# Performance work log

Measured on AMD Instinct MI355X. Metric: run time of the kernel, lower is better.

Reference implementation:

```python
import jax, jax.numpy as jnp
import numpy as np

B, T, C = 4, 2048, 1024
N_HEAD = 16
HEAD_DIM = C // N_HEAD

def setup_inputs() -> dict:
    key = jax.random.key(0)
    k1, k2, k3 = jax.random.split(key, 3)
    x = jax.random.normal(k1, (B, T, C), dtype=jnp.float32)
    # nn.Linear(C, 3C, bias=False): weight [3C, C], y = x @ W.T
    w_qkv = jax.random.normal(k2, (3 * C, C), dtype=jnp.float32) * (1.0 / np.sqrt(C))
    w_proj = jax.random.normal(k3, (C, C), dtype=jnp.float32) * (1.0 / np.sqrt(C))
    return {"x": x, "w_qkv": w_qkv, "w_proj": w_proj}

def reference(x, w_qkv, w_proj):
    Bx, Tx, Cx = x.shape
    qkv = x @ w_qkv.T  # [B,T,3C]
    q, k, v = jnp.split(qkv, 3, axis=-1)
    def heads(t):
        return t.reshape(Bx, Tx, N_HEAD, HEAD_DIM).transpose(0, 2, 1, 3)  # [B,H,T,D]
    q, k, v = heads(q), heads(k), heads(v)
    scale = HEAD_DIM ** -0.5
    att = jnp.einsum('bhtd,bhsd->bhts', q, k) * scale  # [B,H,T,T]
    causal = jnp.tril(jnp.ones((Tx, Tx), dtype=bool))
    att = jnp.where(causal[None, None], att, -jnp.inf)
    att = jax.nn.softmax(att, axis=-1)
    y = jnp.einsum('bhts,bhsd->bhtd', att, v)  # [B,H,T,D]
    y = y.transpose(0, 2, 1, 3).reshape(Bx, Tx, Cx)
    return y @ w_proj.T
```

## Files before the change

### kernel.cpp

```cpp
#include <hip/hip_runtime.h>
#include <hip/hip_bf16.h>

typedef __attribute__((ext_vector_type(8))) short bf16x8;
typedef __attribute__((ext_vector_type(4))) float f32x4;
typedef __attribute__((ext_vector_type(4))) unsigned short ushort4v;
typedef __attribute__((ext_vector_type(2))) unsigned uint2v;

__device__ __forceinline__ unsigned short f2bf(float f) {
  union { float f; unsigned u; } v; v.f = f;
  unsigned r = v.u + 0x7FFFu + ((v.u >> 16) & 1u);
  return (unsigned short)(r >> 16);
}

__device__ __forceinline__ unsigned pack_bf2(float lo, float hi) {
  __hip_bfloat162 h = __float22bfloat162_rn(make_float2(lo, hi));
  union { __hip_bfloat162 h; unsigned u; } cv; cv.h = h; return cv.u;
}

__device__ __forceinline__ void gll16(const void* g, void* l) {
  __builtin_amdgcn_global_load_lds((const __attribute__((address_space(1))) void*)g,
                                   (__attribute__((address_space(3))) void*)l, 16, 0, 0);
}

#define MFMA16(a, b, c) __builtin_amdgcn_mfma_f32_16x16x32_bf16((a), (b), (c), 0, 0, 0)

__global__ void cvt_f32_bf16(const float* __restrict__ s, unsigned short* __restrict__ d, int n) {
  int i = (blockIdx.x * blockDim.x + threadIdx.x) * 4;
  if (i >= n) return;
  float4 f = *(const float4*)(s + i);
  ushort4v r;
  r[0] = f2bf(f.x); r[1] = f2bf(f.y); r[2] = f2bf(f.z); r[3] = f2bf(f.w);
  *(ushort4v*)(d + i) = r;
}

template<int EPI>
__global__ __launch_bounds__(512, 1)
void gemm8(const unsigned short* __restrict__ A,
           const unsigned short* __restrict__ B,
           unsigned short* __restrict__ obf,
           float* __restrict__ of32,
           int M, int N, int K) {
  extern __shared__ unsigned short lds[];
  const int tid = threadIdx.x, wid = tid >> 6, lane = tid & 63;
  const int c = lane & 15, g = lane >> 4;
  const int wr = wid >> 1, wc = wid & 1;
  const int nbn = N >> 7;
  const int nwg = gridDim.x;
  const int wg = (blockIdx.x & 7) * (nwg >> 3) + (blockIdx.x >> 3);
  const int m0 = (wg / nbn) * 256, n0 = (wg % nbn) * 128;
  const int NT = K >> 6;
  const size_t rb = (size_t)K * 2;
  const int sw = (c & 7) << 4;

  const int r8 = lane >> 3;
  const char* Ag = (const char*)A + (size_t)(m0 + r8) * rb + (((lane & 7) ^ r8) * 16);
  const char* Bg = (const char*)B + (size_t)(n0 + r8) * rb + (((lane & 7) ^ r8) * 16);

  auto stageA = [&](int t, int par) {
#pragma unroll
    for (int j = 0; j < 4; ++j) {
      int ch = wid * 4 + j;
      gll16(Ag + (size_t)(ch * 8) * rb + t * 128, lds + par * 16384 + ch * 512);
    }
  };
  auto stageB = [&](int t, int par) {
#pragma unroll
    for (int j = 0; j < 2; ++j) {
      int ch = wid * 2 + j;
      gll16(Bg + (size_t)(ch * 8) * rb + t * 128, lds + 32768 + par * 8192 + ch * 512);
    }
  };

  f32x4 acc[4][4];
#pragma unroll
  for (int i = 0; i < 4; ++i)
#pragma unroll
    for (int j = 0; j < 4; ++j) acc[i][j] = f32x4{0.f, 0.f, 0.f, 0.f};

  stageA(0, 0); stageB(0, 0); stageA(1, 1); stageB(1, 1);
  asm volatile("s_waitcnt vmcnt(4)" ::: "memory");
  __builtin_amdgcn_s_barrier();

  for (int t = 0; t < NT; ++t) {
    const int cur = t & 1;
    const char* Ac = (const char*)(lds + cur * 16384);
    const char* Bc = (const char*)(lds + 32768 + cur * 8192);
    bf16x8 af[4][2], bf0[2][2];
#pragma unroll
    for (int mi = 0; mi < 4; ++mi) {
      int arow = wr * 64 + mi * 16 + c;
#pragma unroll
      for (int kk = 0; kk < 2; ++kk)
        af[mi][kk] = *(const bf16x8*)(Ac + arow * 128 + ((kk * 64 + g * 16) ^ sw));
    }
#pragma unroll
    for (int ni = 0; ni < 2; ++ni) {
      int brow = wc * 64 + ni * 16 + c;
#pragma unroll
      for (int kk = 0; kk < 2; ++kk)
        bf0[ni][kk] = *(const bf16x8*)(Bc + brow * 128 + ((kk * 64 + g * 16) ^ sw));
    }
    if (t + 1 < NT) stageB(t + 1, cur ^ 1);
    __builtin_amdgcn_s_barrier();
    asm volatile("s_waitcnt lgkmcnt(0)" ::: "memory");
    __builtin_amdgcn_sched_barrier(0);
    __builtin_amdgcn_s_setprio(1);
#pragma unroll
    for (int kk = 0; kk < 2; ++kk)
#pragma unroll
      for (int mi = 0; mi < 4; ++mi)
#pragma unroll
        for (int ni = 0; ni < 2; ++ni)
          acc[mi][ni] = MFMA16(bf0[ni][kk], af[mi][kk], acc[mi][ni]);
    __builtin_amdgcn_s_setprio(0);
    __builtin_amdgcn_s_barrier();
    bf16x8 bf1[2][2];
#pragma unroll
    for (int ni = 0; ni < 2; ++ni) {
      int brow = wc * 64 + (ni + 2) * 16 + c;
#pragma unroll
      for (int kk = 0; kk < 2; ++kk)
        bf1[ni][kk] = *(const bf16x8*)(Bc + brow * 128 + ((kk * 64 + g * 16) ^ sw));
    }
    if (t + 2 < NT) stageA(t + 2, cur);
    __builtin_amdgcn_s_barrier();
    asm volatile("s_waitcnt lgkmcnt(0)" ::: "memory");
    __builtin_amdgcn_sched_barrier(0);
    __builtin_amdgcn_s_setprio(1);
#pragma unroll
    for (int kk = 0; kk < 2; ++kk)
#pragma unroll
      for (int mi = 0; mi < 4; ++mi)
#pragma unroll
        for (int ni = 0; ni < 2; ++ni)
          acc[mi][ni + 2] = MFMA16(bf1[ni][kk], af[mi][kk], acc[mi][ni + 2]);
    __builtin_amdgcn_s_setprio(0);
    if (t + 2 < NT) { asm volatile("s_waitcnt vmcnt(4)" ::: "memory"); }
    else            { asm volatile("s_waitcnt vmcnt(0)" ::: "memory"); }
    __builtin_amdgcn_s_barrier();
  }

#pragma unroll
  for (int mi = 0; mi < 4; ++mi) {
    int mg = m0 + wr * 64 + mi * 16 + c;
    if (EPI == 0) {
      int bb = mg >> 11, tt = mg & 2047;
      size_t rowbase = ((size_t)(bb * 16) * 2048 + tt) * 64;
#pragma unroll
      for (int ni = 0; ni < 4; ++ni) {
        int ng = n0 + wc * 64 + ni * 16 + g * 4;
        int which = ng >> 10, rem = ng & 1023;
        int hh = rem >> 6, dd = rem & 63;
        uint2v pk;
        pk[0] = pack_bf2(acc[mi][ni][0], acc[mi][ni][1]);
        pk[1] = pack_bf2(acc[mi][ni][2], acc[mi][ni][3]);
        *(uint2v*)(obf + (size_t)which * 8388608u + rowbase + (size_t)hh * 131072 + dd) = pk;
      }
    } else {
      float* orow = of32 + (size_t)mg * N + n0 + wc * 64 + g * 4;
#pragma unroll
      for (int ni = 0; ni < 4; ++ni)
        *(f32x4*)(orow + ni * 16) = acc[mi][ni];
    }
  }
}

__global__ __launch_bounds__(256, 6)
void attn_fwd(const unsigned short* __restrict__ qb,
              const unsigned short* __restrict__ kb,
              const unsigned short* __restrict__ vb,
              unsigned short* __restrict__ yb) {
  __shared__ unsigned short Kt[64 * 64];
  __shared__ unsigned short Vt[64 * 64];
  __shared__ unsigned short Pl[4 * 16 * 72];
  const int tid = threadIdx.x, w = tid >> 6, lane = tid & 63;
  const int c = lane & 15, g = lane >> 4;
  const int bh = blockIdx.x & 63;
  const int qt = 31 - (blockIdx.x >> 6);
  const int q0 = qt * 64;
  const int b = bh >> 4, h = bh & 15;
  const size_t hb = (size_t)bh * 131072;
  const float GAM = 0.125f * 1.44269504089f;

  const unsigned short* qp = qb + hb + (size_t)(q0 + w * 16 + c) * 64;
  bf16x8 qf0 = *(const bf16x8*)(qp + g * 8);
  bf16x8 qf1 = *(const bf16x8*)(qp + 32 + g * 8);

  f32x4 yacc[4];
#pragma unroll
  for (int i = 0; i < 4; ++i) yacc[i] = f32x4{0.f, 0.f, 0.f, 0.f};
  float mrun = -1e30f, lsum = 0.f;
  unsigned short* pw = Pl + w * (16 * 72);

  for (int kv = 0; kv <= qt; ++kv) {
    const int kv0 = kv * 64;
    const bool diag = (kv == qt);
    if (kv) __syncthreads();
#pragma unroll
    for (int r = 0; r < 2; ++r) {
      int chunk = w * 2 + r;
      int row = chunk * 8 + (lane >> 3);
      int bo = (lane & 7) * 16;
      int sbo = bo ^ ((row & 7) << 4);
      gll16((const char*)(kb + hb + (size_t)(kv0 + row) * 64) + sbo, Kt + chunk * 512);
    }
    {
      int kv2 = (lane & 31) * 2;
      int dblk = w * 16 + (lane >> 5) * 8;
      const unsigned short* vp = vb + hb + (size_t)(kv0 + kv2) * 64 + dblk;
      bf16x8 r0 = *(const bf16x8*)(vp);
      bf16x8 r1 = *(const bf16x8*)(vp + 64);
#pragma unroll
      for (int i = 0; i < 8; ++i) {
        int d = dblk + i;
        unsigned pk2 = ((unsigned)(unsigned short)r0[i]) | (((unsigned)(unsigned short)r1[i]) << 16);
        *(unsigned*)(Vt + d * 64 + (kv2 ^ ((d & 7) << 3))) = pk2;
      }
    }
    __syncthreads();

    f32x4 sacc[4];
#pragma unroll
    for (int nt = 0; nt < 4; ++nt) sacc[nt] = f32x4{0.f, 0.f, 0.f, 0.f};
#pragma unroll
    for (int kk = 0; kk < 2; ++kk)
#pragma unroll
      for (int nt = 0; nt < 4; ++nt) {
        int row = nt * 16 + c;
        bf16x8 kf = *(const bf16x8*)(Kt + row * 64 + ((kk * 32 + g * 8) ^ ((row & 7) << 3)));
        sacc[nt] = MFMA16(kf, (kk ? qf1 : qf0), sacc[nt]);
      }

    if (diag) {
      int ql = w * 16 + c;
#pragma unroll
      for (int nt = 0; nt < 4; ++nt)
#pragma unroll
        for (int r = 0; r < 4; ++r)
          if (nt * 16 + g * 4 + r > ql) sacc[nt][r] = -1e30f;
    }

    float m0 = -1e30f;
#pragma unroll
    for (int nt = 0; nt < 4; ++nt) {
      float a = fmaxf(fmaxf(sacc[nt][0], sacc[nt][1]), fmaxf(sacc[nt][2], sacc[nt][3]));
      m0 = fmaxf(m0, a);
    }
    m0 = fmaxf(m0, __shfl_xor(m0, 16));
    m0 = fmaxf(m0, __shfl_xor(m0, 32));

    if (__any(m0 > mrun + 32.0f)) {
      float mnew = fmaxf(mrun, m0);
      float corr = __builtin_amdgcn_exp2f(GAM * (mrun - mnew));
      lsum *= corr;
#pragma unroll
      for (int dt = 0; dt < 4; ++dt) yacc[dt] *= corr;
      mrun = mnew;
    }

    float bexp = -GAM * mrun;
    float psum = 0.f;
#pragma unroll
    for (int nt = 0; nt < 4; ++nt) {
      float p0 = __builtin_amdgcn_exp2f(fmaf(sacc[nt][0], GAM, bexp));
      float p1 = __builtin_amdgcn_exp2f(fmaf(sacc[nt][1], GAM, bexp));
      float p2 = __builtin_amdgcn_exp2f(fmaf(sacc[nt][2], GAM, bexp));
      float p3 = __builtin_amdgcn_exp2f(fmaf(sacc[nt][3], GAM, bexp));
      psum += (p0 + p1) + (p2 + p3);
      uint2v pkv;
      pkv[0] = pack_bf2(p0, p1);
      pkv[1] = pack_bf2(p2, p3);
      *(uint2v*)(pw + c * 72 + nt * 16 + g * 4) = pkv;
    }
    lsum += psum;

#pragma unroll
    for (int kk = 0; kk < 2; ++kk) {
      bf16x8 pb = *(const bf16x8*)(pw + c * 72 + kk * 32 + g * 8);
#pragma unroll
      for (int dt = 0; dt < 4; ++dt) {
        int n = dt * 16 + c;
        bf16x8 vf = *(const bf16x8*)(Vt + n * 64 + ((kk * 32 + g * 8) ^ ((n & 7) << 3)));
        yacc[dt] = MFMA16(vf, pb, yacc[dt]);
      }
    }
  }

  lsum += __shfl_xor(lsum, 16);
  lsum += __shfl_xor(lsum, 32);
  float inv = 1.0f / lsum;
  int row = q0 + w * 16 + c;
  unsigned short* yp = yb + ((size_t)(b * 2048 + row)) * 1024 + h * 64;
#pragma unroll
  for (int dt = 0; dt < 4; ++dt) {
    uint2v pkv;
    pkv[0] = pack_bf2(yacc[dt][0] * inv, yacc[dt][1] * inv);
    pkv[1] = pack_bf2(yacc[dt][2] * inv, yacc[dt][3] * inv);
    *(uint2v*)(yp + dt * 16 + g * 4) = pkv;
  }
}

extern "C" void kernel_launch(void* const* d_in, const int* in_sizes, int n_in,
                              void* d_out, int out_size, void* d_ws, size_t ws_size,
                              hipStream_t stream) {
  const float* x     = (const float*)d_in[0];
  const float* wqkv  = (const float*)d_in[1];
  const float* wproj = (const float*)d_in[2];
  float* out = (float*)d_out;

  unsigned short* ws     = (unsigned short*)d_ws;
  unsigned short* xb     = ws;
  unsigned short* wqkvb  = xb + 8388608;
  unsigned short* wprojb = wqkvb + 3145728;
  unsigned short* qkvb   = wprojb + 1048576;
  unsigned short* yb     = qkvb + 3 * 8388608;

  cvt_f32_bf16<<<8192, 256, 0, stream>>>(x, xb, 8388608);
  cvt_f32_bf16<<<3072, 256, 0, stream>>>(wqkv, wqkvb, 3145728);
  cvt_f32_bf16<<<1024, 256, 0, stream>>>(wproj, wprojb, 1048576);

  gemm8<0><<<768, 512, 98304, stream>>>(xb, wqkvb, qkvb, nullptr, 8192, 3072, 1024);
  attn_fwd<<<2048, 256, 0, stream>>>(qkvb, qkvb + 8388608, qkvb + 2 * 8388608, yb);
  gemm8<1><<<256, 512, 98304, stream>>>(yb, wprojb, nullptr, out, 8192, 1024, 1024);
}
```

Measured before the change: 179.5 us.

## Make QKV GEMM persistent with cross-tile prefetch; compute softmax denominator via MFMA

The QKV GEMM becomes a persistent kernel: 256 blocks each process three output tiles and prefetch the next tile's first K-slices during the current tile's tail, hiding the prologue and epilogue. The attention kernel drops the scalar row-sum of probabilities. It instead runs one extra MFMA against a ones matrix in LDS to get the softmax denominator, and XOR-swizzles the P buffer instead of padding it. This trades some extra MFMA work and an LDS ones tile for fewer VALU adds and shuffles, and the persistent GEMM risks imbalance since 768 tiles over 256 CUs is even only if all CUs are free.

```diff
diff --git a/kernel.cpp b/kernel.cpp
--- a/kernel.cpp
+++ b/kernel.cpp
@@ -33,9 +33,9 @@
   *(ushort4v*)(d + i) = r;
 }
 
-template<int EPI>
+template<int EPI, int RPB>
 __global__ __launch_bounds__(512, 1)
-void gemm8(const unsigned short* __restrict__ A,
+void gemmp(const unsigned short* __restrict__ A,
            const unsigned short* __restrict__ B,
            unsigned short* __restrict__ obf,
            float* __restrict__ of32,
@@ -45,29 +45,30 @@
   const int c = lane & 15, g = lane >> 4;
   const int wr = wid >> 1, wc = wid & 1;
   const int nbn = N >> 7;
-  const int nwg = gridDim.x;
-  const int wg = (blockIdx.x & 7) * (nwg >> 3) + (blockIdx.x >> 3);
-  const int m0 = (wg / nbn) * 256, n0 = (wg % nbn) * 128;
+  const int swzbid = (blockIdx.x & 7) * (gridDim.x >> 3) + (blockIdx.x >> 3);
   const int NT = K >> 6;
   const size_t rb = (size_t)K * 2;
   const int sw = (c & 7) << 4;
 
-  const int r8 = lane >> 3;
-  const char* Ag = (const char*)A + (size_t)(m0 + r8) * rb + (((lane & 7) ^ r8) * 16);
-  const char* Bg = (const char*)B + (size_t)(n0 + r8) * rb + (((lane & 7) ^ r8) * 16);
-
-  auto stageA = [&](int t, int par) {
+  const int srow = lane >> 3;
+  const int sslot = (lane & 7) ^ srow;
+  const char* Abase = (const char*)A;
+  const char* Bbase = (const char*)B;
+
+  auto stageA = [&](int m0p, int kt, int par) {
+    const char* Agp = Abase + (size_t)(m0p + srow) * rb + sslot * 16 + kt * 128;
 #pragma unroll
     for (int j = 0; j < 4; ++j) {
       int ch = wid * 4 + j;
-      gll16(Ag + (size_t)(ch * 8) * rb + t * 128, lds + par * 16384 + ch * 512);
+      gll16(Agp + (size_t)(ch * 8) * rb, lds + par * 16384 + ch * 512);
     }
   };
-  auto stageB = [&](int t, int par) {
+  auto stageB = [&](int n0p, int kt, int par) {
+    const char* Bgp = Bbase + (size_t)(n0p + srow) * rb + sslot * 16 + kt * 128;
 #pragma unroll
     for (int j = 0; j < 2; ++j) {
       int ch = wid * 2 + j;
-      gll16(Bg + (size_t)(ch * 8) * rb + t * 128, lds + 32768 + par * 8192 + ch * 512);
+      gll16(Bgp + (size_t)(ch * 8) * rb, lds + 32768 + par * 8192 + ch * 512);
     }
   };
 
@@ -77,91 +78,116 @@
 #pragma unroll
     for (int j = 0; j < 4; ++j) acc[i][j] = f32x4{0.f, 0.f, 0.f, 0.f};
 
-  stageA(0, 0); stageB(0, 0); stageA(1, 1); stageB(1, 1);
+  int m0c = (swzbid / nbn) * 256, n0c = (swzbid % nbn) * 128;
+
+  stageA(m0c, 0, 0); stageB(n0c, 0, 0); stageA(m0c, 1, 1); stageB(n0c, 1, 1);
   asm volatile("s_waitcnt vmcnt(4)" ::: "memory");
   __builtin_amdgcn_s_barrier();
 
-  for (int t = 0; t < NT; ++t) {
-    const int cur = t & 1;
-    const char* Ac = (const char*)(lds + cur * 16384);
-    const char* Bc = (const char*)(lds + 32768 + cur * 8192);
-    bf16x8 af[4][2], bf0[2][2];
+  for (int p = 0; p < RPB; ++p) {
+    int m0n = 0, n0n = 0;
+    const bool morep = (p + 1 < RPB);
+    if (morep) {
+      int tile = (p + 1) * gridDim.x + swzbid;
+      m0n = (tile / nbn) * 256; n0n = (tile % nbn) * 128;
+    }
+    for (int t = 0; t < NT; ++t) {
+      const int par = t & 1;
+      const char* Ac = (const char*)(lds + par * 16384);
+      const char* Bc = (const char*)(lds + 32768 + par * 8192);
+      bf16x8 af[4][2], bf0[2][2];
+#pragma unroll
+      for (int mi = 0; mi < 4; ++mi) {
+        int arow = wr * 64 + mi * 16 + c;
+#pragma unroll
+        for (int kk = 0; kk < 2; ++kk)
+          af[mi][kk] = *(const bf16x8*)(Ac + arow * 128 + ((kk * 64 + g * 16) ^ sw));
+      }
+#pragma unroll
+      for (int ni = 0; ni < 2; ++ni) {
+        int brow = wc * 64 + ni * 16 + c;
+#pragma unroll
+        for (int kk = 0; kk < 2; ++kk)
+          bf0[ni][kk] = *(const bf16x8*)(Bc + brow * 128 + ((kk * 64 + g * 16) ^ sw));
+      }
+      {
+        int tB = t + 1;
+        if (tB < NT)      stageB(n0c, tB, tB & 1);
+        else if (morep)   stageB(n0n, tB - NT, tB & 1);
+      }
+      __builtin_amdgcn_s_barrier();
+      asm volatile("s_waitcnt lgkmcnt(0)" ::: "memory");
+      __builtin_amdgcn_sched_barrier(0);
+      __builtin_amdgcn_s_setprio(1);
+#pragma unroll
+      for (int kk = 0; kk < 2; ++kk)
+#pragma unroll
+        for (int mi = 0; mi < 4; ++mi)
+#pragma unroll
+          for (int ni = 0; ni < 2; ++ni)
+            acc[mi][ni] = MFMA16(bf0[ni][kk], af[mi][kk], acc[mi][ni]);
+      __builtin_amdgcn_s_setprio(0);
+      __builtin_amdgcn_s_barrier();
+      bf16x8 bf1[2][2];
+#pragma unroll
+      for (int ni = 0; ni < 2; ++ni) {
+        int brow = wc * 64 + (ni + 2) * 16 + c;
+#pragma unroll
+        for (int kk = 0; kk < 2; ++kk)
+          bf1[ni][kk] = *(const bf16x8*)(Bc + brow * 128 + ((kk * 64 + g * 16) ^ sw));
+      }
+      bool okA;
+      {
+        int tA = t + 2;
+        okA = (tA < NT) || morep;
+        if (tA < NT)      stageA(m0c, tA, tA & 1);
+        else if (morep)   stageA(m0n, tA - NT, tA & 1);
+      }
+      __builtin_amdgcn_s_barrier();
+      asm volatile("s_waitcnt lgkmcnt(0)" ::: "memory");
+      __builtin_amdgcn_sched_barrier(0);
+      __builtin_amdgcn_s_setprio(1);
+#pragma unroll
+      for (int kk = 0; kk < 2; ++kk)
+#pragma unroll
+        for (int mi = 0; mi < 4; ++mi)
+#pragma unroll
+          for (int ni = 0; ni < 2; ++ni)
+            acc[mi][ni + 2] = MFMA16(bf1[ni][kk], af[mi][kk], acc[mi][ni + 2]);
+      __builtin_amdgcn_s_setprio(0);
+      if (okA) { asm volatile("s_waitcnt vmcnt(4)" ::: "memory"); }
+      else     { asm volatile("s_waitcnt vmcnt(0)" ::: "memory"); }
+      __builtin_amdgcn_s_barrier();
+    }
+
 #pragma unroll
     for (int mi = 0; mi < 4; ++mi) {
-      int arow = wr * 64 + mi * 16 + c;
-#pragma unroll
-      for (int kk = 0; kk < 2; ++kk)
-        af[mi][kk] = *(const bf16x8*)(Ac + arow * 128 + ((kk * 64 + g * 16) ^ sw));
-    }
-#pragma unroll
-    for (int ni = 0; ni < 2; ++ni) {
-      int brow = wc * 64 + ni * 16 + c;
-#pragma unroll
-      for (int kk = 0; kk < 2; ++kk)
-        bf0[ni][kk] = *(const bf16x8*)(Bc + brow * 128 + ((kk * 64 + g * 16) ^ sw));
-    }
-    if (t + 1 < NT) stageB(t + 1, cur ^ 1);
-    __builtin_amdgcn_s_barrier();
-    asm volatile("s_waitcnt lgkmcnt(0)" ::: "memory");
-    __builtin_amdgcn_sched_barrier(0);
-    __builtin_amdgcn_s_setprio(1);
-#pragma unroll
-    for (int kk = 0; kk < 2; ++kk)
-#pragma unroll
-      for (int mi = 0; mi < 4; ++mi)
-#pragma unroll
-        for (int ni = 0; ni < 2; ++ni)
-          acc[mi][ni] = MFMA16(bf0[ni][kk], af[mi][kk], acc[mi][ni]);
-    __builtin_amdgcn_s_setprio(0);
-    __builtin_amdgcn_s_barrier();
-    bf16x8 bf1[2][2];
-#pragma unroll
-    for (int ni = 0; ni < 2; ++ni) {
-      int brow = wc * 64 + (ni + 2) * 16 + c;
-#pragma unroll
-      for (int kk = 0; kk < 2; ++kk)
-        bf1[ni][kk] = *(const bf16x8*)(Bc + brow * 128 + ((kk * 64 + g * 16) ^ sw));
-    }
-    if (t + 2 < NT) stageA(t + 2, cur);
-    __builtin_amdgcn_s_barrier();
-    asm volatile("s_waitcnt lgkmcnt(0)" ::: "memory");
-    __builtin_amdgcn_sched_barrier(0);
-    __builtin_amdgcn_s_setprio(1);
-#pragma unroll
-    for (int kk = 0; kk < 2; ++kk)
-#pragma unroll
-      for (int mi = 0; mi < 4; ++mi)
-#pragma unroll
-        for (int ni = 0; ni < 2; ++ni)
-          acc[mi][ni + 2] = MFMA16(bf1[ni][kk], af[mi][kk], acc[mi][ni + 2]);
-    __builtin_amdgcn_s_setprio(0);
-    if (t + 2 < NT) { asm volatile("s_waitcnt vmcnt(4)" ::: "memory"); }
-    else            { asm volatile("s_waitcnt vmcnt(0)" ::: "memory"); }
-    __builtin_amdgcn_s_barrier();
-  }
-
-#pragma unroll
-  for (int mi = 0; mi < 4; ++mi) {
-    int mg = m0 + wr * 64 + mi * 16 + c;
-    if (EPI == 0) {
-      int bb = mg >> 11, tt = mg & 2047;
-      size_t rowbase = ((size_t)(bb * 16) * 2048 + tt) * 64;
-#pragma unroll
-      for (int ni = 0; ni < 4; ++ni) {
-        int ng = n0 + wc * 64 + ni * 16 + g * 4;
-        int which = ng >> 10, rem = ng & 1023;
-        int hh = rem >> 6, dd = rem & 63;
-        uint2v pk;
-        pk[0] = pack_bf2(acc[mi][ni][0], acc[mi][ni][1]);
-        pk[1] = pack_bf2(acc[mi][ni][2], acc[mi][ni][3]);
-        *(uint2v*)(obf + (size_t)which * 8388608u + rowbase + (size_t)hh * 131072 + dd) = pk;
-      }
-    } else {
-      float* orow = of32 + (size_t)mg * N + n0 + wc * 64 + g * 4;
-#pragma unroll
-      for (int ni = 0; ni < 4; ++ni)
-        *(f32x4*)(orow + ni * 16) = acc[mi][ni];
-    }
+      int mg = m0c + wr * 64 + mi * 16 + c;
+      if (EPI == 0) {
+        int bb = mg >> 11, tt = mg & 2047;
+        size_t rowbase = ((size_t)(bb * 16) * 2048 + tt) * 64;
+#pragma unroll
+        for (int ni = 0; ni < 4; ++ni) {
+          int ng = n0c + wc * 64 + ni * 16 + g * 4;
+          int which = ng >> 10, rem = ng & 1023;
+          int hh = rem >> 6, dd = rem & 63;
+          uint2v pk;
+          pk[0] = pack_bf2(acc[mi][ni][0], acc[mi][ni][1]);
+          pk[1] = pack_bf2(acc[mi][ni][2], acc[mi][ni][3]);
+          *(uint2v*)(obf + (size_t)which * 8388608u + rowbase + (size_t)hh * 131072 + dd) = pk;
+        }
+      } else {
+        float* orow = of32 + (size_t)mg * N + n0c + wc * 64 + g * 4;
+#pragma unroll
+        for (int ni = 0; ni < 4; ++ni)
+          *(f32x4*)(orow + ni * 16) = acc[mi][ni];
+      }
+    }
+#pragma unroll
+    for (int i = 0; i < 4; ++i)
+#pragma unroll
+      for (int j = 0; j < 4; ++j) acc[i][j] = f32x4{0.f, 0.f, 0.f, 0.f};
+    m0c = m0n; n0c = n0n;
   }
 }
 
@@ -172,7 +198,8 @@
               unsigned short* __restrict__ yb) {
   __shared__ unsigned short Kt[64 * 64];
   __shared__ unsigned short Vt[64 * 64];
-  __shared__ unsigned short Pl[4 * 16 * 72];
+  __shared__ unsigned short Pl[4 * 16 * 64];
+  __shared__ unsigned short Ones[16 * 64];
   const int tid = threadIdx.x, w = tid >> 6, lane = tid & 63;
   const int c = lane & 15, g = lane >> 4;
   const int bh = blockIdx.x & 63;
@@ -181,16 +208,23 @@
   const int b = bh >> 4, h = bh & 15;
   const size_t hb = (size_t)bh * 131072;
   const float GAM = 0.125f * 1.44269504089f;
+  const int psw = (c & 7) << 3;
+
+  {
+    ushort4v z; unsigned short v1 = (tid < 16) ? (unsigned short)0x3F80 : (unsigned short)0;
+    z[0] = v1; z[1] = v1; z[2] = v1; z[3] = v1;
+    *(ushort4v*)(Ones + tid * 4) = z;
+  }
 
   const unsigned short* qp = qb + hb + (size_t)(q0 + w * 16 + c) * 64;
   bf16x8 qf0 = *(const bf16x8*)(qp + g * 8);
   bf16x8 qf1 = *(const bf16x8*)(qp + 32 + g * 8);
 
-  f32x4 yacc[4];
-#pragma unroll
-  for (int i = 0; i < 4; ++i) yacc[i] = f32x4{0.f, 0.f, 0.f, 0.f};
-  float mrun = -1e30f, lsum = 0.f;
-  unsigned short* pw = Pl + w * (16 * 72);
+  f32x4 yacc[5];
+#pragma unroll
+  for (int i = 0; i < 5; ++i) yacc[i] = f32x4{0.f, 0.f, 0.f, 0.f};
+  float mrun = -1e30f;
+  unsigned short* pw = Pl + w * 1024;
 
   for (int kv = 0; kv <= qt; ++kv) {
     const int kv0 = kv * 64;
@@ -252,43 +286,40 @@
     if (__any(m0 > mrun + 32.0f)) {
       float mnew = fmaxf(mrun, m0);
       float corr = __builtin_amdgcn_exp2f(GAM * (mrun - mnew));
-      lsum *= corr;
-#pragma unroll
-      for (int dt = 0; dt < 4; ++dt) yacc[dt] *= corr;
+#pragma unroll
+      for (int dt = 0; dt < 5; ++dt) yacc[dt] *= corr;
       mrun = mnew;
     }
 
     float bexp = -GAM * mrun;
-    float psum = 0.f;
 #pragma unroll
     for (int nt = 0; nt < 4; ++nt) {
       float p0 = __builtin_amdgcn_exp2f(fmaf(sacc[nt][0], GAM, bexp));
       float p1 = __builtin_amdgcn_exp2f(fmaf(sacc[nt][1], GAM, bexp));
       float p2 = __builtin_amdgcn_exp2f(fmaf(sacc[nt][2], GAM, bexp));
       float p3 = __builtin_amdgcn_exp2f(fmaf(sacc[nt][3], GAM, bexp));
-      psum += (p0 + p1) + (p2 + p3);
       uint2v pkv;
       pkv[0] = pack_bf2(p0, p1);
       pkv[1] = pack_bf2(p2, p3);
-      *(uint2v*)(pw + c * 72 + nt * 16 + g * 4) = pkv;
-    }
-    lsum += psum;
+      *(uint2v*)(pw + c * 64 + ((nt * 16 + g * 4) ^ psw)) = pkv;
+    }
 
 #pragma unroll
     for (int kk = 0; kk < 2; ++kk) {
-      bf16x8 pb = *(const bf16x8*)(pw + c * 72 + kk * 32 + g * 8);
+      bf16x8 pb = *(const bf16x8*)(pw + c * 64 + ((kk * 32 + g * 8) ^ psw));
 #pragma unroll
       for (int dt = 0; dt < 4; ++dt) {
         int n = dt * 16 + c;
         bf16x8 vf = *(const bf16x8*)(Vt + n * 64 + ((kk * 32 + g * 8) ^ ((n & 7) << 3)));
         yacc[dt] = MFMA16(vf, pb, yacc[dt]);
       }
+      bf16x8 of = *(const bf16x8*)(Ones + c * 64 + ((kk * 32 + g * 8) ^ psw));
+      yacc[4] = MFMA16(of, pb, yacc[4]);
     }
   }
 
-  lsum += __shfl_xor(lsum, 16);
-  lsum += __shfl_xor(lsum, 32);
-  float inv = 1.0f / lsum;
+  float ls = __shfl(yacc[4][0], c);
+  float inv = 1.0f / ls;
   int row = q0 + w * 16 + c;
   unsigned short* yp = yb + ((size_t)(b * 2048 + row)) * 1024 + h * 64;
 #pragma unroll
@@ -319,7 +350,7 @@
   cvt_f32_bf16<<<3072, 256, 0, stream>>>(wqkv, wqkvb, 3145728);
   cvt_f32_bf16<<<1024, 256, 0, stream>>>(wproj, wprojb, 1048576);
 
-  gemm8<0><<<768, 512, 98304, stream>>>(xb, wqkvb, qkvb, nullptr, 8192, 3072, 1024);
+  gemmp<0, 3><<<256, 512, 98304, stream>>>(xb, wqkvb, qkvb, nullptr, 8192, 3072, 1024);
   attn_fwd<<<2048, 256, 0, stream>>>(qkvb, qkvb + 8388608, qkvb + 2 * 8388608, yb);
-  gemm8<1><<<256, 512, 98304, stream>>>(yb, wprojb, nullptr, out, 8192, 1024, 1024);
-}
+  gemmp<1, 1><<<256, 512, 98304, stream>>>(yb, wprojb, nullptr, out, 8192, 1024, 1024);
+}
```

New measurement: 201.7 us. +12.3%, slower.
